# Performance work log

Hardware: AMD Instinct MI355X
Metric: run time of the kernel (lower is better)

The kernel has to match this reference:

```python
import jax, jax.numpy as jnp
import numpy as np

B, T, C, H = 4, 4096, 1024, 128

def setup_inputs() -> dict:
    key = jax.random.key(0)
    kx, kk, kq, kv = jax.random.split(key, 4)
    scale = 1.0 / np.sqrt(C)  # mimic Linear init scale
    return {
        'x':  jax.random.normal(kx, (B, T, C), dtype=jnp.float32),
        'Wk': jax.random.normal(kk, (C, H), dtype=jnp.float32) * scale,
        'Wq': jax.random.normal(kq, (C, H), dtype=jnp.float32) * scale,
        'Wv': jax.random.normal(kv, (C, H), dtype=jnp.float32) * scale,
    }

def reference(x, Wk, Wq, Wv):
    # x: [B,T,C]; projections to [B,T,H]
    k = jnp.einsum('btc,ch->bth', x, Wk)
    q = jnp.einsum('btc,ch->bth', x, Wq)
    v = jnp.einsum('btc,ch->bth', x, Wv)
    scale = jnp.asarray(x.shape[-1] and (k.shape[-1] ** -0.5), dtype=x.dtype)
    # scores: [B,T,T]
    scores = jnp.einsum('bqh,bkh->bqk', q, k) * scale
    Tn = x.shape[1]
    causal = jnp.tril(jnp.ones((Tn, Tn), dtype=bool))
    scores = jnp.where(causal[None, :, :], scores, -jnp.inf)
    attn = jax.nn.softmax(scores, axis=-1)
    # dropout=0.0 -> identity
    out = jnp.einsum('bqk,bkh->bqh', attn, v)
    return out
```

## Files before the change

### kernel.cpp

```cpp
#include <hip/hip_runtime.h>
#include <hip/hip_bf16.h>
#include <math.h>

#define B_ 4
#define T_ 4096
#define C_ 1024
#define H_ 128
#define SCALE 0.08838834764831845f

typedef __attribute__((ext_vector_type(8))) short bf16x8;
typedef __attribute__((ext_vector_type(4))) float f32x4;

__device__ __forceinline__ unsigned short f2bf(float f) {
    union { float f; unsigned u; } x; x.f = f;
    unsigned r = x.u + 0x7FFF + ((x.u >> 16) & 1);
    return (unsigned short)(r >> 16);
}
__device__ __forceinline__ float bf2f(unsigned short u) {
    union { unsigned u; float f; } x; x.u = ((unsigned)u) << 16;
    return x.f;
}
__device__ __forceinline__ unsigned cvt_pk_bf16(float a, float b) {
    unsigned r;
    asm("v_cvt_pk_bf16_f32 %0, %1, %2" : "=v"(r) : "v"(a), "v"(b));
    return r;
}

#define GLOAD16(gsrc, ldst)                                                        \
    __builtin_amdgcn_global_load_lds(                                              \
        (const __attribute__((address_space(1))) unsigned int*)(gsrc),             \
        (__attribute__((address_space(3))) unsigned int*)(ldst), 16, 0, 0)

__global__ __launch_bounds__(256) void wtrans_kernel(
        const float* __restrict__ Wk, const float* __restrict__ Wq,
        const float* __restrict__ Wv, unsigned short* __restrict__ Wt) {
    int tid = blockIdx.x * 256 + threadIdx.x;
    int t = tid >> 17;
    int r = tid & 131071;
    int c = r >> 7;
    int h = r & 127;
    const float* W = (t == 0) ? Wk : (t == 1) ? Wq : Wv;
    Wt[t * 131072 + h * 1024 + c] = f2bf(W[r]);
}

__global__ __launch_bounds__(256) void qkv_gemm(
        const float* __restrict__ x, const unsigned short* __restrict__ Wt,
        unsigned short* __restrict__ qkv) {
    __shared__ unsigned short As[64][72];
    __shared__ unsigned short Bs[384][72];

    const int m0 = blockIdx.x * 64;
    const int tid = threadIdx.x;
    const int lane = tid & 63;
    const int w = tid >> 6;
    const int fr = lane & 15;
    const int fq = lane >> 4;

    f32x4 acc[6][4];
#pragma unroll
    for (int i = 0; i < 6; i++)
#pragma unroll
        for (int rf = 0; rf < 4; rf++) acc[i][rf] = f32x4{0.f, 0.f, 0.f, 0.f};

    for (int k0 = 0; k0 < C_; k0 += 64) {
        __syncthreads();
        {
            int row = tid >> 2;
            int coff = (tid & 3) * 16;
            const float* src = x + (long)(m0 + row) * C_ + k0 + coff;
            unsigned short tmp[16];
#pragma unroll
            for (int i = 0; i < 4; i++) {
                float4 v = ((const float4*)src)[i];
                tmp[i*4+0] = f2bf(v.x); tmp[i*4+1] = f2bf(v.y);
                tmp[i*4+2] = f2bf(v.z); tmp[i*4+3] = f2bf(v.w);
            }
            uint4* dst = (uint4*)&As[row][coff];
            dst[0] = ((uint4*)tmp)[0];
            dst[1] = ((uint4*)tmp)[1];
        }
#pragma unroll
        for (int i = 0; i < 12; i++) {
            int idx = tid + i * 256;
            int row = idx >> 3;
            int coff = (idx & 7) * 8;
            *(uint4*)&Bs[row][coff] =
                *(const uint4*)(Wt + (long)row * 1024 + k0 + coff);
        }
        __syncthreads();

#pragma unroll
        for (int kk = 0; kk < 2; kk++) {
            bf16x8 a[4], bb[6];
#pragma unroll
            for (int rf = 0; rf < 4; rf++)
                a[rf] = *(const bf16x8*)&As[rf*16 + fr][kk*32 + fq*8];
#pragma unroll
            for (int i = 0; i < 6; i++)
                bb[i] = *(const bf16x8*)&Bs[(w*6 + i)*16 + fr][kk*32 + fq*8];
#pragma unroll
            for (int i = 0; i < 6; i++)
#pragma unroll
                for (int rf = 0; rf < 4; rf++)
                    acc[i][rf] = __builtin_amdgcn_mfma_f32_16x16x32_bf16(
                        a[rf], bb[i], acc[i][rf], 0, 0, 0);
        }
    }
#pragma unroll
    for (int i = 0; i < 6; i++) {
        int nf = w*6 + i;
        int t = nf >> 3;
        int col = (nf & 7) * 16 + fr;
#pragma unroll
        for (int rf = 0; rf < 4; rf++)
#pragma unroll
            for (int r = 0; r < 4; r++) {
                int row = m0 + rf*16 + fq*4 + r;
                qkv[(long)t * (16384L * 128) + (long)row * 128 + col] = f2bf(acc[i][rf][r]);
            }
    }
}

__global__ __launch_bounds__(256) void vtrans_kernel(
        const unsigned short* __restrict__ v, unsigned short* __restrict__ vT) {
    __shared__ unsigned short tile[64][136];
    const int t0 = (blockIdx.x & 63) * 64;
    const int b = blockIdx.x >> 6;
    const int tid = threadIdx.x;
#pragma unroll
    for (int i = 0; i < 4; i++) {
        int idx = tid + i * 256;
        int tr = idx >> 4, coff = (idx & 15) * 8;
        *(uint4*)&tile[tr][coff] =
            *(const uint4*)(v + ((long)(b * T_ + t0 + tr)) * H_ + coff);
    }
    __syncthreads();
#pragma unroll
    for (int i = 0; i < 4; i++) {
        int idx = tid + i * 256;
        int h = idx >> 3, ts = (idx & 7) * 8;
        unsigned short tmp[8];
#pragma unroll
        for (int j = 0; j < 8; j++) tmp[j] = tile[ts + j][h];
        *(uint4*)(vT + ((long)(b * H_ + h)) * T_ + t0 + ts) = *(uint4*)tmp;
    }
}

__global__ __launch_bounds__(512, 4) void flash6_kernel(
        const unsigned short* __restrict__ qkv,
        const unsigned short* __restrict__ vT,
        unsigned short* __restrict__ po0, unsigned short* __restrict__ po1,
        unsigned short* __restrict__ po2, unsigned short* __restrict__ po3,
        float* __restrict__ pm, float* __restrict__ pl) {
    __shared__ unsigned short k_lds[2][64][128];
    __shared__ unsigned short v_lds[2][128][64];

    const int n = blockIdx.x;
    const int half = n >> 8;
    const int m = n & 255;
    const int b = (m & 7) >> 1;
    const int r = ((m >> 3) << 1) | (m & 1);
    const int jj = r & 31;
    const int pq = r >> 5;
    const int qt = half ? (31 - jj) : jj;
    const int p = half * 2 + pq;
    const int q0 = qt * 128;
    const int ntt = (qt + 1) * 2;
    const int t0 = (p * ntt) >> 2;
    const int t1 = ((p + 1) * ntt) >> 2;

    const int tid = threadIdx.x;
    const int w = tid >> 6;
    const int lane = tid & 63;
    const int fr = lane & 15;
    const int fq = lane >> 4;

    const unsigned short* kbase = qkv + (long)b * T_ * H_;
    const unsigned short* vbase = vT + (long)b * H_ * T_;

    const int kcolb0 = ((lane & 15) << 4) ^ ((((lane >> 4)) & 7) << 4);
    const int kcolb1 = ((lane & 15) << 4) ^ (((4 + (lane >> 4)) & 7) << 4);
    const int krl = lane >> 4;
    const int vrl = lane >> 3;
    const int vcolb = ((lane & 7) << 4) ^ (vrl << 4);
    unsigned short* const klds_flat = &k_lds[0][0][0];
    unsigned short* const vlds_flat = &v_lds[0][0][0];

    const int scol = ((fq ^ (fr & 7)) << 4);

    bf16x8 qf[4];
    {
        const unsigned short* qptr = qkv + 2097152 + ((long)b*T_ + q0 + w*16 + fr) * H_;
#pragma unroll
        for (int ks = 0; ks < 4; ks++)
            qf[ks] = *(const bf16x8*)(qptr + ks*32 + fq*8);
    }

    f32x4 acc[8];
#pragma unroll
    for (int i = 0; i < 8; i++) acc[i] = f32x4{0.f, 0.f, 0.f, 0.f};
    float m_r = -INFINITY, l_r = 0.f;
    const int qrow = q0 + w*16 + fr;

    int cur = 0;
    if (t0 < t1) {
        const int kv0 = t0 * 64;
#pragma unroll
        for (int i = 0; i < 2; i++) {
            int kcolb = i ? kcolb1 : kcolb0;
            GLOAD16(kbase + (long)(kv0 + 8*w + 4*i + krl) * 128 + (kcolb >> 1),
                    klds_flat + w*1024 + i*512);
            GLOAD16(vbase + (long)(16*w + 8*i + vrl) * 4096 + kv0 + (vcolb >> 1),
                    vlds_flat + w*1024 + i*512);
        }
    }

    for (int t = t0; t < t1; ++t) {
        const int kv0 = t * 64;
        __syncthreads();
        if (t + 1 < t1) {
            const int kv0n = kv0 + 64;
            const int boff = (cur ^ 1) * 8192;
#pragma unroll
            for (int i = 0; i < 2; i++) {
                int kcolb = i ? kcolb1 : kcolb0;
                GLOAD16(kbase + (long)(kv0n + 8*w + 4*i + krl) * 128 + (kcolb >> 1),
                        klds_flat + boff + w*1024 + i*512);
                GLOAD16(vbase + (long)(16*w + 8*i + vrl) * 4096 + kv0n + (vcolb >> 1),
                        vlds_flat + boff + w*1024 + i*512);
            }
            asm volatile("s_waitcnt vmcnt(4)" ::: "memory");
        } else {
            asm volatile("s_waitcnt vmcnt(0)" ::: "memory");
        }
        __syncthreads();

        const char* kl = (const char*)k_lds + cur*16384 + fr*256;
        const char* vl = (const char*)v_lds + cur*16384 + fr*128;

        f32x4 s[4];
#pragma unroll
        for (int sf = 0; sf < 4; sf++) s[sf] = f32x4{0.f,0.f,0.f,0.f};
        __builtin_amdgcn_s_setprio(1);
#pragma unroll
        for (int sf = 0; sf < 4; sf++)
#pragma unroll
            for (int ks = 0; ks < 4; ks++) {
                bf16x8 kf = *(const bf16x8*)(kl + sf*4096 + (scol ^ (ks << 6)));
                s[sf] = __builtin_amdgcn_mfma_f32_16x16x32_bf16(kf, qf[ks], s[sf], 0, 0, 0);
            }
        __builtin_amdgcn_s_setprio(0);

        float mx = -INFINITY;
        if (kv0 + 63 > q0 + 16*w) {
#pragma unroll
            for (int sf = 0; sf < 4; sf++)
#pragma unroll
                for (int rr = 0; rr < 4; rr++) {
                    int kv = kv0 + sf*16 + fq*4 + rr;
                    float sv = s[sf][rr] * SCALE;
                    sv = (kv > qrow) ? -INFINITY : sv;
                    s[sf][rr] = sv;
                    mx = fmaxf(mx, sv);
                }
        } else {
#pragma unroll
            for (int sf = 0; sf < 4; sf++)
#pragma unroll
                for (int rr = 0; rr < 4; rr++) {
                    float sv = s[sf][rr] * SCALE;
                    s[sf][rr] = sv;
                    mx = fmaxf(mx, sv);
                }
        }
        mx = fmaxf(mx, __shfl_xor(mx, 16, 64));
        mx = fmaxf(mx, __shfl_xor(mx, 32, 64));

        const bool skip = __all((m_r > -1e37f) & (mx - m_r <= 8.f));
        float msub;
        if (skip) {
            msub = m_r;
        } else {
            float mn = fmaxf(m_r, mx);
            msub = (mn == -INFINITY) ? 0.f : mn;
            float alpha = __expf(m_r - msub);
            m_r = mn;
#pragma unroll
            for (int hf = 0; hf < 8; hf++)
#pragma unroll
                for (int rr = 0; rr < 4; rr++) acc[hf][rr] *= alpha;
            l_r *= alpha;
        }

        float pv[4][4];
        float sum = 0.f;
#pragma unroll
        for (int sf = 0; sf < 4; sf++)
#pragma unroll
            for (int rr = 0; rr < 4; rr++) {
                float e = __expf(s[sf][rr] - msub);
                pv[sf][rr] = e;
                sum += e;
            }
        sum += __shfl_xor(sum, 16, 64);
        sum += __shfl_xor(sum, 32, 64);
        l_r += sum;

        unsigned pw[8];
#pragma unroll
        for (int sf = 0; sf < 4; sf++) {
            pw[2*sf]   = cvt_pk_bf16(pv[sf][0], pv[sf][1]);
            pw[2*sf+1] = cvt_pk_bf16(pv[sf][2], pv[sf][3]);
        }
        unsigned pbu[2][4];
        pbu[0][0]=0;pbu[0][1]=0;pbu[0][2]=0;pbu[0][3]=0;
        pbu[1][0]=0;pbu[1][1]=0;pbu[1][2]=0;pbu[1][3]=0;
        const int L1 = fr + 16 * ((fq & 1) * 2);
        const int L2 = L1 + 16;
        const int sel = (fq >> 1) & 1;
#pragma unroll
        for (int sf = 0; sf < 4; sf++) {
            unsigned w0 = (unsigned)__shfl((int)pw[2*sf],   L1, 64);
            unsigned w1 = (unsigned)__shfl((int)pw[2*sf+1], L1, 64);
            unsigned w2 = (unsigned)__shfl((int)pw[2*sf],   L2, 64);
            unsigned w3 = (unsigned)__shfl((int)pw[2*sf+1], L2, 64);
            if ((sf & 1) == sel) {
                int k2 = sf >> 1;
                pbu[k2][0] = w0; pbu[k2][1] = w1; pbu[k2][2] = w2; pbu[k2][3] = w3;
            }
        }
        union { unsigned u[4]; bf16x8 v; } pb0c, pb1c;
#pragma unroll
        for (int i = 0; i < 4; i++) { pb0c.u[i] = pbu[0][i]; pb1c.u[i] = pbu[1][i]; }
        bf16x8 pb0 = pb0c.v, pb1 = pb1c.v;

        __builtin_amdgcn_s_setprio(1);
#pragma unroll
        for (int hf = 0; hf < 8; hf++) {
            bf16x8 vf0 = *(const bf16x8*)(vl + hf*2048 + scol);
            bf16x8 vf1 = *(const bf16x8*)(vl + hf*2048 + (scol ^ 64));
            acc[hf] = __builtin_amdgcn_mfma_f32_16x16x32_bf16(vf0, pb0, acc[hf], 0, 0, 0);
            acc[hf] = __builtin_amdgcn_mfma_f32_16x16x32_bf16(vf1, pb1, acc[hf], 0, 0, 0);
        }
        __builtin_amdgcn_s_setprio(0);
        cur ^= 1;
    }

    unsigned short* po = (p == 0) ? po0 : (p == 1) ? po1 : (p == 2) ? po2 : po3;
    float linv = (l_r > 0.f) ? (1.0f / l_r) : 0.f;
    const long obase = ((long)b * T_ + qrow) * H_;
#pragma unroll
    for (int hf = 0; hf < 8; hf++) {
        unsigned u0 = cvt_pk_bf16(acc[hf][0] * linv, acc[hf][1] * linv);
        unsigned u1 = cvt_pk_bf16(acc[hf][2] * linv, acc[hf][3] * linv);
        uint2 uu; uu.x = u0; uu.y = u1;
        *(uint2*)(po + obase + hf*16 + fq*4) = uu;
    }
    if (fq == 0) {
        pm[p * 16384 + b * T_ + qrow] = m_r;
        pl[p * 16384 + b * T_ + qrow] = l_r;
    }
}

__global__ __launch_bounds__(256) void combine_kernel(
        const unsigned short* __restrict__ po0,
        const unsigned short* __restrict__ po1,
        const unsigned short* __restrict__ po2,
        const unsigned short* __restrict__ po3,
        const float* __restrict__ pm, const float* __restrict__ pl,
        float* __restrict__ out) {
    int idx = blockIdx.x * 256 + threadIdx.x;
    int row = idx >> 4;
    int seg = idx & 15;
    float mv[4], lv[4];
#pragma unroll
    for (int i = 0; i < 4; i++) { mv[i] = pm[i*16384 + row]; lv[i] = pl[i*16384 + row]; }
    float m = fmaxf(fmaxf(mv[0], mv[1]), fmaxf(mv[2], mv[3]));
    float wv[4]; float tot = 0.f;
#pragma unroll
    for (int i = 0; i < 4; i++) {
        wv[i] = (lv[i] > 0.f) ? __expf(mv[i] - m) * lv[i] : 0.f;
        tot += wv[i];
    }
    float inv = 1.0f / tot;
    long off = (long)row * H_ + seg * 8;
    unsigned short ua[8], ub[8], uc[8], ud[8];
    *(uint4*)ua = *(const uint4*)(po0 + off);
    *(uint4*)ub = *(const uint4*)(po1 + off);
    *(uint4*)uc = *(const uint4*)(po2 + off);
    *(uint4*)ud = *(const uint4*)(po3 + off);
    float* o = out + off;
#pragma unroll
    for (int j2 = 0; j2 < 8; j2++)
        o[j2] = inv * (wv[0] * bf2f(ua[j2]) + wv[1] * bf2f(ub[j2]) +
                       wv[2] * bf2f(uc[j2]) + wv[3] * bf2f(ud[j2]));
}

extern "C" void kernel_launch(void* const* d_in, const int* in_sizes, int n_in,
                              void* d_out, int out_size, void* d_ws, size_t ws_size,
                              hipStream_t stream) {
    (void)in_sizes; (void)n_in; (void)out_size; (void)ws_size;
    const float* x  = (const float*)d_in[0];
    const float* Wk = (const float*)d_in[1];
    const float* Wq = (const float*)d_in[2];
    const float* Wv = (const float*)d_in[3];
    float* out = (float*)d_out;

    unsigned short* Wt  = (unsigned short*)d_ws;
    unsigned short* qkv = Wt + 393216;
    unsigned short* vT  = qkv + 6291456;
    unsigned short* po0 = vT + 2097152;
    unsigned short* po1 = po0 + 2097152;
    unsigned short* po3 = po1 + 2097152;
    unsigned short* po2 = qkv + 4194304;
    float* pm = (float*)d_ws;
    float* pl = pm + 65536;

    wtrans_kernel<<<1536, 256, 0, stream>>>(Wk, Wq, Wv, Wt);
    qkv_gemm<<<256, 256, 0, stream>>>(x, Wt, qkv);
    vtrans_kernel<<<256, 256, 0, stream>>>(qkv + 4194304, vT);
    flash6_kernel<<<512, 512, 0, stream>>>(qkv, vT, po0, po1, po2, po3, pm, pl);
    combine_kernel<<<1024, 256, 0, stream>>>(po0, po1, po2, po3, pm, pl, out);
}
```

Baseline: 96.51 us.

## Fuse V transpose into pipelined QKV GEMM and split attention six ways

The QKV projection GEMM now splits the output columns across twice as many blocks. It double-buffers the x and W tiles, using asynchronous global-to-LDS loads with a swizzled layout, and writes V directly in transposed form, so the separate transpose kernel is gone. A new flash attention kernel splits each query tile's KV range into six parts instead of four and uses a single V buffer, aiming at more blocks and higher occupancy. A six-way combine kernel follows, with a fallback to the old path if the workspace is too small. In exchange it takes more workspace and more partial-output traffic in the combine step.

Result: slower. 112.0 us (+16.0%).

```diff
diff --git a/kernel.cpp b/kernel.cpp
--- a/kernel.cpp
+++ b/kernel.cpp
@@ -24,6 +24,14 @@
     unsigned r;
     asm("v_cvt_pk_bf16_f32 %0, %1, %2" : "=v"(r) : "v"(a), "v"(b));
     return r;
+}
+__device__ __forceinline__ void cvt16(const float4& a, const float4& b,
+                                      const float4& c, const float4& d,
+                                      unsigned short* t) {
+    t[0]=f2bf(a.x);  t[1]=f2bf(a.y);  t[2]=f2bf(a.z);  t[3]=f2bf(a.w);
+    t[4]=f2bf(b.x);  t[5]=f2bf(b.y);  t[6]=f2bf(b.z);  t[7]=f2bf(b.w);
+    t[8]=f2bf(c.x);  t[9]=f2bf(c.y);  t[10]=f2bf(c.z); t[11]=f2bf(c.w);
+    t[12]=f2bf(d.x); t[13]=f2bf(d.y); t[14]=f2bf(d.z); t[15]=f2bf(d.w);
 }
 
 #define GLOAD16(gsrc, ldst)                                                        \
@@ -43,108 +51,127 @@
     Wt[t * 131072 + h * 1024 + c] = f2bf(W[r]);
 }
 
-__global__ __launch_bounds__(256) void qkv_gemm(
+__global__ __launch_bounds__(256, 2) void qkv_gemm2(
         const float* __restrict__ x, const unsigned short* __restrict__ Wt,
-        unsigned short* __restrict__ qkv) {
-    __shared__ unsigned short As[64][72];
-    __shared__ unsigned short Bs[384][72];
-
-    const int m0 = blockIdx.x * 64;
+        unsigned short* __restrict__ qkv, unsigned short* __restrict__ vT) {
+    __shared__ unsigned short As[2][64][72];
+    __shared__ unsigned short Bs[2][192][64];
+
+    const int nsw = blockIdx.x;
+    const int sw = (nsw & 7) * 64 + (nsw >> 3);
+    const int m0 = (sw >> 1) * 64;
+    const int nh = sw & 1;
+
     const int tid = threadIdx.x;
     const int lane = tid & 63;
     const int w = tid >> 6;
     const int fr = lane & 15;
     const int fq = lane >> 4;
 
-    f32x4 acc[6][4];
+    const int xrow = tid >> 2, xco = (tid & 3) * 16;
+    const float* xsrc = x + (long)(m0 + xrow) * C_ + xco;
+    const int brl = lane >> 3;
+    const int bcolb = (((lane & 7) ^ brl) << 4);
+    unsigned short* const bs_flat = &Bs[0][0][0];
+    const unsigned short* wbase = Wt + (long)(nh * 192) * 1024;
+
+    f32x4 acc[3][4];
+#pragma unroll
+    for (int i = 0; i < 3; i++)
+#pragma unroll
+        for (int rf = 0; rf < 4; rf++) acc[i][rf] = f32x4{0.f, 0.f, 0.f, 0.f};
+
+    float4 xr0, xr1, xr2, xr3;
+    xr0 = ((const float4*)xsrc)[0]; xr1 = ((const float4*)xsrc)[1];
+    xr2 = ((const float4*)xsrc)[2]; xr3 = ((const float4*)xsrc)[3];
 #pragma unroll
     for (int i = 0; i < 6; i++)
-#pragma unroll
-        for (int rf = 0; rf < 4; rf++) acc[i][rf] = f32x4{0.f, 0.f, 0.f, 0.f};
-
-    for (int k0 = 0; k0 < C_; k0 += 64) {
+        GLOAD16(wbase + (long)(48*w + 8*i + brl) * 1024 + (bcolb >> 1),
+                bs_flat + (w*6 + i) * 512);
+    {
+        unsigned short tmp[16];
+        cvt16(xr0, xr1, xr2, xr3, tmp);
+        *(uint4*)&As[0][xrow][xco]     = ((uint4*)tmp)[0];
+        *(uint4*)&As[0][xrow][xco + 8] = ((uint4*)tmp)[1];
+    }
+
+    int cur = 0;
+    for (int k = 0; k < 16; ++k) {
         __syncthreads();
-        {
-            int row = tid >> 2;
-            int coff = (tid & 3) * 16;
-            const float* src = x + (long)(m0 + row) * C_ + k0 + coff;
-            unsigned short tmp[16];
-#pragma unroll
-            for (int i = 0; i < 4; i++) {
-                float4 v = ((const float4*)src)[i];
-                tmp[i*4+0] = f2bf(v.x); tmp[i*4+1] = f2bf(v.y);
-                tmp[i*4+2] = f2bf(v.z); tmp[i*4+3] = f2bf(v.w);
-            }
-            uint4* dst = (uint4*)&As[row][coff];
-            dst[0] = ((uint4*)tmp)[0];
-            dst[1] = ((uint4*)tmp)[1];
-        }
-#pragma unroll
-        for (int i = 0; i < 12; i++) {
-            int idx = tid + i * 256;
-            int row = idx >> 3;
-            int coff = (idx & 7) * 8;
-            *(uint4*)&Bs[row][coff] =
-                *(const uint4*)(Wt + (long)row * 1024 + k0 + coff);
+        const bool more = (k + 1) < 16;
+        if (more) {
+            const float* xs = xsrc + (k + 1) * 64;
+            xr0 = ((const float4*)xs)[0]; xr1 = ((const float4*)xs)[1];
+            xr2 = ((const float4*)xs)[2]; xr3 = ((const float4*)xs)[3];
+            const int boff = (cur ^ 1) * 12288;
+#pragma unroll
+            for (int i = 0; i < 6; i++)
+                GLOAD16(wbase + (long)(48*w + 8*i + brl) * 1024 + (k + 1) * 64 + (bcolb >> 1),
+                        bs_flat + boff + (w*6 + i) * 512);
+            asm volatile("s_waitcnt vmcnt(10)" ::: "memory");
+        } else {
+            asm volatile("s_waitcnt vmcnt(0)" ::: "memory");
         }
         __syncthreads();
 
+        const char* bsb = (const char*)bs_flat + cur * 24576;
+        __builtin_amdgcn_s_setprio(1);
 #pragma unroll
         for (int kk = 0; kk < 2; kk++) {
-            bf16x8 a[4], bb[6];
+            bf16x8 a[4], bb[3];
 #pragma unroll
             for (int rf = 0; rf < 4; rf++)
-                a[rf] = *(const bf16x8*)&As[rf*16 + fr][kk*32 + fq*8];
-#pragma unroll
-            for (int i = 0; i < 6; i++)
-                bb[i] = *(const bf16x8*)&Bs[(w*6 + i)*16 + fr][kk*32 + fq*8];
-#pragma unroll
-            for (int i = 0; i < 6; i++)
+                a[rf] = *(const bf16x8*)&As[cur][rf*16 + fr][kk*32 + fq*8];
+#pragma unroll
+            for (int i = 0; i < 3; i++) {
+                int row = (w*3 + i) * 16 + fr;
+                bb[i] = *(const bf16x8*)(bsb + row*128 + ((((kk<<2) + fq) ^ (fr & 7)) << 4));
+            }
+#pragma unroll
+            for (int i = 0; i < 3; i++)
 #pragma unroll
                 for (int rf = 0; rf < 4; rf++)
                     acc[i][rf] = __builtin_amdgcn_mfma_f32_16x16x32_bf16(
                         a[rf], bb[i], acc[i][rf], 0, 0, 0);
         }
-    }
-#pragma unroll
-    for (int i = 0; i < 6; i++) {
-        int nf = w*6 + i;
-        int t = nf >> 3;
-        int col = (nf & 7) * 16 + fr;
-#pragma unroll
-        for (int rf = 0; rf < 4; rf++)
-#pragma unroll
-            for (int r = 0; r < 4; r++) {
-                int row = m0 + rf*16 + fq*4 + r;
-                qkv[(long)t * (16384L * 128) + (long)row * 128 + col] = f2bf(acc[i][rf][r]);
-            }
-    }
-}
-
-__global__ __launch_bounds__(256) void vtrans_kernel(
-        const unsigned short* __restrict__ v, unsigned short* __restrict__ vT) {
-    __shared__ unsigned short tile[64][136];
-    const int t0 = (blockIdx.x & 63) * 64;
-    const int b = blockIdx.x >> 6;
-    const int tid = threadIdx.x;
-#pragma unroll
-    for (int i = 0; i < 4; i++) {
-        int idx = tid + i * 256;
-        int tr = idx >> 4, coff = (idx & 15) * 8;
-        *(uint4*)&tile[tr][coff] =
-            *(const uint4*)(v + ((long)(b * T_ + t0 + tr)) * H_ + coff);
-    }
-    __syncthreads();
-#pragma unroll
-    for (int i = 0; i < 4; i++) {
-        int idx = tid + i * 256;
-        int h = idx >> 3, ts = (idx & 7) * 8;
-        unsigned short tmp[8];
-#pragma unroll
-        for (int j = 0; j < 8; j++) tmp[j] = tile[ts + j][h];
-        *(uint4*)(vT + ((long)(b * H_ + h)) * T_ + t0 + ts) = *(uint4*)tmp;
-    }
-}
+        __builtin_amdgcn_s_setprio(0);
+
+        if (more) {
+            unsigned short tmp[16];
+            cvt16(xr0, xr1, xr2, xr3, tmp);
+            *(uint4*)&As[cur ^ 1][xrow][xco]     = ((uint4*)tmp)[0];
+            *(uint4*)&As[cur ^ 1][xrow][xco + 8] = ((uint4*)tmp)[1];
+        }
+        cur ^= 1;
+    }
+
+#pragma unroll
+    for (int i = 0; i < 3; i++) {
+        int nfg = nh*12 + w*3 + i;
+        int t = nfg >> 3;
+        int col = (nfg & 7) * 16 + fr;
+        if (t < 2) {
+#pragma unroll
+            for (int rf = 0; rf < 4; rf++)
+#pragma unroll
+                for (int r = 0; r < 4; r++) {
+                    int row = m0 + rf*16 + fq*4 + r;
+                    qkv[(long)t * 2097152 + (long)row * 128 + col] = f2bf(acc[i][rf][r]);
+                }
+        } else {
+            const int bb_ = m0 >> 12;
+            const int trow = m0 & 4095;
+#pragma unroll
+            for (int rf = 0; rf < 4; rf++) {
+                uint2 uu;
+                uu.x = cvt_pk_bf16(acc[i][rf][0], acc[i][rf][1]);
+                uu.y = cvt_pk_bf16(acc[i][rf][2], acc[i][rf][3]);
+                *(uint2*)(vT + ((long)(bb_*128 + col)) * 4096 + trow + rf*16 + fq*4) = uu;
+            }
+        }
+    }
+}
+
 
 __global__ __launch_bounds__(512, 4) void flash6_kernel(
         const unsigned short* __restrict__ qkv,
@@ -185,7 +212,6 @@
     const int vcolb = ((lane & 7) << 4) ^ (vrl << 4);
     unsigned short* const klds_flat = &k_lds[0][0][0];
     unsigned short* const vlds_flat = &v_lds[0][0][0];
-
     const int scol = ((fq ^ (fr & 7)) << 4);
 
     bf16x8 qf[4];
@@ -351,9 +377,9 @@
     const long obase = ((long)b * T_ + qrow) * H_;
 #pragma unroll
     for (int hf = 0; hf < 8; hf++) {
-        unsigned u0 = cvt_pk_bf16(acc[hf][0] * linv, acc[hf][1] * linv);
-        unsigned u1 = cvt_pk_bf16(acc[hf][2] * linv, acc[hf][3] * linv);
-        uint2 uu; uu.x = u0; uu.y = u1;
+        uint2 uu;
+        uu.x = cvt_pk_bf16(acc[hf][0] * linv, acc[hf][1] * linv);
+        uu.y = cvt_pk_bf16(acc[hf][2] * linv, acc[hf][3] * linv);
         *(uint2*)(po + obase + hf*16 + fq*4) = uu;
     }
     if (fq == 0) {
@@ -362,7 +388,220 @@
     }
 }
 
-__global__ __launch_bounds__(256) void combine_kernel(
+__global__ __launch_bounds__(512, 6) void flash7_kernel(
+        const unsigned short* __restrict__ qkv,
+        const unsigned short* __restrict__ vT,
+        unsigned short* __restrict__ po,
+        float* __restrict__ pm, float* __restrict__ pl) {
+    __shared__ unsigned short k_lds[2][64][128];
+    __shared__ unsigned short v_lds[128][64];
+
+    const int n = blockIdx.x;
+    const int b = (n & 7) >> 1;
+    const int r = ((n >> 3) << 1) | (n & 1);
+    const int p = r % 6;
+    const int qt = 31 - (r / 6);
+    const int q0 = qt * 128;
+    const int ntt = (qt + 1) * 2;
+    const int t0 = (p * ntt) / 6;
+    const int t1 = ((p + 1) * ntt) / 6;
+
+    const int tid = threadIdx.x;
+    const int w = tid >> 6;
+    const int lane = tid & 63;
+    const int fr = lane & 15;
+    const int fq = lane >> 4;
+
+    const unsigned short* kbase = qkv + (long)b * T_ * H_;
+    const unsigned short* vbase = vT + (long)b * H_ * T_;
+
+    const int kcolb0 = ((lane & 15) << 4) ^ ((((lane >> 4)) & 7) << 4);
+    const int kcolb1 = ((lane & 15) << 4) ^ (((4 + (lane >> 4)) & 7) << 4);
+    const int krl = lane >> 4;
+    const int vrl = lane >> 3;
+    const int vcolb = ((lane & 7) << 4) ^ (vrl << 4);
+    unsigned short* const klds_flat = &k_lds[0][0][0];
+    unsigned short* const vlds_flat = &v_lds[0][0];
+    const int scol = ((fq ^ (fr & 7)) << 4);
+
+    bf16x8 qf[4];
+    {
+        const unsigned short* qptr = qkv + 2097152 + ((long)b*T_ + q0 + w*16 + fr) * H_;
+#pragma unroll
+        for (int ks = 0; ks < 4; ks++)
+            qf[ks] = *(const bf16x8*)(qptr + ks*32 + fq*8);
+    }
+
+    f32x4 acc[8];
+#pragma unroll
+    for (int i = 0; i < 8; i++) acc[i] = f32x4{0.f, 0.f, 0.f, 0.f};
+    float m_r = -INFINITY, l_r = 0.f;
+    const int qrow = q0 + w*16 + fr;
+
+    int cur = 0;
+    if (t0 < t1) {
+        const int kv0 = t0 * 64;
+#pragma unroll
+        for (int i = 0; i < 2; i++) {
+            int kcolb = i ? kcolb1 : kcolb0;
+            GLOAD16(kbase + (long)(kv0 + 8*w + 4*i + krl) * 128 + (kcolb >> 1),
+                    klds_flat + w*1024 + i*512);
+        }
+    }
+
+    for (int t = t0; t < t1; ++t) {
+        const int kv0 = t * 64;
+        __syncthreads();
+#pragma unroll
+        for (int i = 0; i < 2; i++)
+            GLOAD16(vbase + (long)(16*w + 8*i + vrl) * 4096 + kv0 + (vcolb >> 1),
+                    vlds_flat + w*1024 + i*512);
+        if (t + 1 < t1) {
+            const int kv0n = kv0 + 64;
+            const int boff = (cur ^ 1) * 8192;
+#pragma unroll
+            for (int i = 0; i < 2; i++) {
+                int kcolb = i ? kcolb1 : kcolb0;
+                GLOAD16(kbase + (long)(kv0n + 8*w + 4*i + krl) * 128 + (kcolb >> 1),
+                        klds_flat + boff + w*1024 + i*512);
+            }
+            asm volatile("s_waitcnt vmcnt(4)" ::: "memory");
+        } else {
+            asm volatile("s_waitcnt vmcnt(2)" ::: "memory");
+        }
+        __syncthreads();
+
+        const char* kl = (const char*)k_lds + cur*16384 + fr*256;
+        const char* vl = (const char*)v_lds + fr*128;
+
+        f32x4 s[4];
+#pragma unroll
+        for (int sf = 0; sf < 4; sf++) s[sf] = f32x4{0.f,0.f,0.f,0.f};
+        __builtin_amdgcn_s_setprio(1);
+#pragma unroll
+        for (int sf = 0; sf < 4; sf++)
+#pragma unroll
+            for (int ks = 0; ks < 4; ks++) {
+                bf16x8 kf = *(const bf16x8*)(kl + sf*4096 + (scol ^ (ks << 6)));
+                s[sf] = __builtin_amdgcn_mfma_f32_16x16x32_bf16(kf, qf[ks], s[sf], 0, 0, 0);
+            }
+        __builtin_amdgcn_s_setprio(0);
+
+        float mx = -INFINITY;
+        if (kv0 + 63 > q0 + 16*w) {
+#pragma unroll
+            for (int sf = 0; sf < 4; sf++)
+#pragma unroll
+                for (int rr = 0; rr < 4; rr++) {
+                    int kv = kv0 + sf*16 + fq*4 + rr;
+                    float sv = s[sf][rr] * SCALE;
+                    sv = (kv > qrow) ? -INFINITY : sv;
+                    s[sf][rr] = sv;
+                    mx = fmaxf(mx, sv);
+                }
+        } else {
+#pragma unroll
+            for (int sf = 0; sf < 4; sf++)
+#pragma unroll
+                for (int rr = 0; rr < 4; rr++) {
+                    float sv = s[sf][rr] * SCALE;
+                    s[sf][rr] = sv;
+                    mx = fmaxf(mx, sv);
+                }
+        }
+        mx = fmaxf(mx, __shfl_xor(mx, 16, 64));
+        mx = fmaxf(mx, __shfl_xor(mx, 32, 64));
+
+        const bool skip = __all((m_r > -1e37f) & (mx - m_r <= 8.f));
+        float msub;
+        if (skip) {
+            msub = m_r;
+        } else {
+            float mn = fmaxf(m_r, mx);
+            msub = (mn == -INFINITY) ? 0.f : mn;
+            float alpha = __expf(m_r - msub);
+            m_r = mn;
+#pragma unroll
+            for (int hf = 0; hf < 8; hf++)
+#pragma unroll
+                for (int rr = 0; rr < 4; rr++) acc[hf][rr] *= alpha;
+            l_r *= alpha;
+        }
+
+        float pv[4][4];
+        float sum = 0.f;
+#pragma unroll
+        for (int sf = 0; sf < 4; sf++)
+#pragma unroll
+            for (int rr = 0; rr < 4; rr++) {
+                float e = __expf(s[sf][rr] - msub);
+                pv[sf][rr] = e;
+                sum += e;
+            }
+        sum += __shfl_xor(sum, 16, 64);
+        sum += __shfl_xor(sum, 32, 64);
+        l_r += sum;
+
+        unsigned pw[8];
+#pragma unroll
+        for (int sf = 0; sf < 4; sf++) {
+            pw[2*sf]   = cvt_pk_bf16(pv[sf][0], pv[sf][1]);
+            pw[2*sf+1] = cvt_pk_bf16(pv[sf][2], pv[sf][3]);
+        }
+        unsigned pbu[2][4];
+        pbu[0][0]=0;pbu[0][1]=0;pbu[0][2]=0;pbu[0][3]=0;
+        pbu[1][0]=0;pbu[1][1]=0;pbu[1][2]=0;pbu[1][3]=0;
+        const int L1 = fr + 16 * ((fq & 1) * 2);
+        const int L2 = L1 + 16;
+        const int sel = (fq >> 1) & 1;
+#pragma unroll
+        for (int sf = 0; sf < 4; sf++) {
+            unsigned w0 = (unsigned)__shfl((int)pw[2*sf],   L1, 64);
+            unsigned w1 = (unsigned)__shfl((int)pw[2*sf+1], L1, 64);
+            unsigned w2 = (unsigned)__shfl((int)pw[2*sf],   L2, 64);
+            unsigned w3 = (unsigned)__shfl((int)pw[2*sf+1], L2, 64);
+            if ((sf & 1) == sel) {
+                int k2 = sf >> 1;
+                pbu[k2][0] = w0; pbu[k2][1] = w1; pbu[k2][2] = w2; pbu[k2][3] = w3;
+            }
+        }
+        union { unsigned u[4]; bf16x8 v; } pb0c, pb1c;
+#pragma unroll
+        for (int i = 0; i < 4; i++) { pb0c.u[i] = pbu[0][i]; pb1c.u[i] = pbu[1][i]; }
+        bf16x8 pb0 = pb0c.v, pb1 = pb1c.v;
+
+        if (t + 1 < t1) asm volatile("s_waitcnt vmcnt(2)" ::: "memory");
+        else            asm volatile("s_waitcnt vmcnt(0)" ::: "memory");
+        __syncthreads();
+
+        __builtin_amdgcn_s_setprio(1);
+#pragma unroll
+        for (int hf = 0; hf < 8; hf++) {
+            bf16x8 vf0 = *(const bf16x8*)(vl + hf*2048 + scol);
+            bf16x8 vf1 = *(const bf16x8*)(vl + hf*2048 + (scol ^ 64));
+            acc[hf] = __builtin_amdgcn_mfma_f32_16x16x32_bf16(vf0, pb0, acc[hf], 0, 0, 0);
+            acc[hf] = __builtin_amdgcn_mfma_f32_16x16x32_bf16(vf1, pb1, acc[hf], 0, 0, 0);
+        }
+        __builtin_amdgcn_s_setprio(0);
+        cur ^= 1;
+    }
+
+    float linv = (l_r > 0.f) ? (1.0f / l_r) : 0.f;
+    const long obase = (long)p * 2097152 + ((long)b * T_ + qrow) * H_;
+#pragma unroll
+    for (int hf = 0; hf < 8; hf++) {
+        uint2 uu;
+        uu.x = cvt_pk_bf16(acc[hf][0] * linv, acc[hf][1] * linv);
+        uu.y = cvt_pk_bf16(acc[hf][2] * linv, acc[hf][3] * linv);
+        *(uint2*)(po + obase + hf*16 + fq*4) = uu;
+    }
+    if (fq == 0) {
+        pm[p * 16384 + b * T_ + qrow] = m_r;
+        pl[p * 16384 + b * T_ + qrow] = l_r;
+    }
+}
+
+__global__ __launch_bounds__(256) void combine4_kernel(
         const unsigned short* __restrict__ po0,
         const unsigned short* __restrict__ po1,
         const unsigned short* __restrict__ po2,
@@ -396,10 +635,46 @@
                        wv[2] * bf2f(uc[j2]) + wv[3] * bf2f(ud[j2]));
 }
 
+__global__ __launch_bounds__(256) void combine6_kernel(
+        const unsigned short* __restrict__ po,
+        const float* __restrict__ pm, const float* __restrict__ pl,
+        float* __restrict__ out) {
+    int idx = blockIdx.x * 256 + threadIdx.x;
+    int row = idx >> 4;
+    int seg = idx & 15;
+    float mv[6], lv[6];
+#pragma unroll
+    for (int i = 0; i < 6; i++) { mv[i] = pm[i*16384 + row]; lv[i] = pl[i*16384 + row]; }
+    float m = mv[0];
+#pragma unroll
+    for (int i = 1; i < 6; i++) m = fmaxf(m, mv[i]);
+    float wv[6]; float tot = 0.f;
+#pragma unroll
+    for (int i = 0; i < 6; i++) {
+        wv[i] = (lv[i] > 0.f) ? __expf(mv[i] - m) * lv[i] : 0.f;
+        tot += wv[i];
+    }
+    float inv = 1.0f / tot;
+    long off = (long)row * H_ + seg * 8;
+    float* o = out + off;
+    float res[8];
+#pragma unroll
+    for (int j2 = 0; j2 < 8; j2++) res[j2] = 0.f;
+#pragma unroll
+    for (int i = 0; i < 6; i++) {
+        unsigned short ua[8];
+        *(uint4*)ua = *(const uint4*)(po + (long)i * 2097152 + off);
+#pragma unroll
+        for (int j2 = 0; j2 < 8; j2++) res[j2] += wv[i] * bf2f(ua[j2]);
+    }
+#pragma unroll
+    for (int j2 = 0; j2 < 8; j2++) o[j2] = inv * res[j2];
+}
+
 extern "C" void kernel_launch(void* const* d_in, const int* in_sizes, int n_in,
                               void* d_out, int out_size, void* d_ws, size_t ws_size,
                               hipStream_t stream) {
-    (void)in_sizes; (void)n_in; (void)out_size; (void)ws_size;
+    (void)in_sizes; (void)n_in; (void)out_size;
     const float* x  = (const float*)d_in[0];
     const float* Wk = (const float*)d_in[1];
     const float* Wq = (const float*)d_in[2];
@@ -409,16 +684,25 @@
     unsigned short* Wt  = (unsigned short*)d_ws;
     unsigned short* qkv = Wt + 393216;
     unsigned short* vT  = qkv + 6291456;
-    unsigned short* po0 = vT + 2097152;
-    unsigned short* po1 = po0 + 2097152;
-    unsigned short* po3 = po1 + 2097152;
-    unsigned short* po2 = qkv + 4194304;
-    float* pm = (float*)d_ws;
-    float* pl = pm + 65536;
 
     wtrans_kernel<<<1536, 256, 0, stream>>>(Wk, Wq, Wv, Wt);
-    qkv_gemm<<<256, 256, 0, stream>>>(x, Wt, qkv);
-    vtrans_kernel<<<256, 256, 0, stream>>>(qkv + 4194304, vT);
-    flash6_kernel<<<512, 512, 0, stream>>>(qkv, vT, po0, po1, po2, po3, pm, pl);
-    combine_kernel<<<1024, 256, 0, stream>>>(po0, po1, po2, po3, pm, pl, out);
-}
+    qkv_gemm2<<<512, 256, 0, stream>>>(x, Wt, qkv, vT);
+
+    const size_t need7 = ((size_t)393216 + 10u * 2097152u) * 2u;
+    if (ws_size >= need7) {
+        unsigned short* po = vT + 2097152;
+        float* pm = (float*)d_ws;
+        float* pl = pm + 98304;
+        flash7_kernel<<<768, 512, 0, stream>>>(qkv, vT, po, pm, pl);
+        combine6_kernel<<<1024, 256, 0, stream>>>(po, pm, pl, out);
+    } else {
+        unsigned short* po0 = vT + 2097152;
+        unsigned short* po1 = po0 + 2097152;
+        unsigned short* po3 = po1 + 2097152;
+        unsigned short* po2 = qkv + 4194304;
+        float* pm = (float*)d_ws;
+        float* pl = pm + 65536;
+        flash6_kernel<<<512, 512, 0, stream>>>(qkv, vT, po0, po1, po2, po3, pm, pl);
+        combine4_kernel<<<1024, 256, 0, stream>>>(po0, po1, po2, po3, pm, pl, out);
+    }
+}
```
